# Performance work log

Measured on AMD Instinct MI355X. Metric: run time of the kernel, lower is better.

Reference implementation:

```python
import jax, jax.numpy as jnp
import numpy as np

N = 50000      # num_nodes
E = 300000     # edges per edge type
T = 3          # num_edge_type
C = 2          # num_channels
F_IN = 64      # feature_size
HID = 64       # hidden_size (w_out)
NL = 2         # num_layers (GT layers per FastGTN)
BETA = 0.5     # gtn_beta
TP = 0.8       # teleport_probability


def setup_inputs() -> dict:
    key = jax.random.key(0)
    ks = jax.random.split(key, 16)
    X = jax.random.normal(ks[0], (N, F_IN), dtype=jnp.float32)
    edge_index_0 = jax.random.randint(ks[1], (2, E), 0, N)
    edge_index_1 = jax.random.randint(ks[2], (2, E), 0, N)
    edge_index_2 = jax.random.randint(ks[3], (2, E), 0, N)
    edge_value_0 = jax.random.uniform(ks[4], (E,), dtype=jnp.float32)
    edge_value_1 = jax.random.uniform(ks[5], (E,), dtype=jnp.float32)
    edge_value_2 = jax.random.uniform(ks[6], (E,), dtype=jnp.float32)
    # glorot for Ws (per-channel projection), std=0.1 for GT layer mixing weights
    g0 = np.sqrt(6.0 / (F_IN + HID))
    g1 = np.sqrt(6.0 / (HID + HID))
    Ws0 = jax.random.uniform(ks[7], (C, F_IN, HID), minval=-g0, maxval=g0, dtype=jnp.float32)
    Ws1 = jax.random.uniform(ks[8], (C, HID, HID), minval=-g1, maxval=g1, dtype=jnp.float32)
    layerW0 = 0.1 * jax.random.normal(ks[9], (NL, C, T), dtype=jnp.float32)
    layerW1 = 0.1 * jax.random.normal(ks[10], (NL, C, T), dtype=jnp.float32)
    gl = np.sqrt(1.0 / (C * HID))
    lin_W0 = jax.random.uniform(ks[11], (C * HID, HID), minval=-gl, maxval=gl, dtype=jnp.float32)
    lin_b0 = jax.random.uniform(ks[12], (HID,), minval=-gl, maxval=gl, dtype=jnp.float32)
    lin_W1 = jax.random.uniform(ks[13], (C * HID, HID), minval=-gl, maxval=gl, dtype=jnp.float32)
    lin_b1 = jax.random.uniform(ks[14], (HID,), minval=-gl, maxval=gl, dtype=jnp.float32)
    return dict(X=X,
                edge_value_0=edge_value_0, edge_value_1=edge_value_1, edge_value_2=edge_value_2,
                Ws0=Ws0, Ws1=Ws1, layerW0=layerW0, layerW1=layerW1,
                lin_W0=lin_W0, lin_b0=lin_b0, lin_W1=lin_W1, lin_b1=lin_b1,
                edge_index_0=edge_index_0, edge_index_1=edge_index_1, edge_index_2=edge_index_2)


def _spmm_mix(H, filt, vals, etype, row, col):
    # H: [C, N, d]; filt: [C, T] softmaxed; vals: [Etot]; etype/row/col: [Etot]
    # == for each channel c: sum_j filt[c,j] * (A_j @ H[c])
    w = vals[None, :] * filt[:, etype]          # [C, Etot]
    msg = w[:, :, None] * H[:, col, :]          # [C, Etot, d]
    return jax.vmap(lambda m: jax.ops.segment_sum(m, row, num_segments=N))(msg)


def _fastgtn_block(Xin, Ws, layerW, linW, linb, row, col, vals, etype):
    H = jnp.einsum('nf,cfo->cno', Xin, Ws)      # [C, N, HID]
    X0 = jax.lax.stop_gradient(H)               # X_ = H.clone().detach()
    for l in range(NL):
        filt = jax.nn.softmax(layerW[l], axis=1)
        H = _spmm_mix(H, filt, vals, etype, row, col)
    Hm = TP * jax.nn.relu(BETA * X0 + (1.0 - BETA) * H) + (1.0 - TP) * X0
    Hm = jnp.transpose(Hm, (1, 0, 2)).reshape(N, C * Hm.shape[-1])  # [N, C*HID]
    return jax.nn.relu(Hm @ linW + linb)


def reference(X, edge_value_0, edge_value_1, edge_value_2,
              Ws0, Ws1, layerW0, layerW1,
              lin_W0, lin_b0, lin_W1, lin_b1,
              edge_index_0, edge_index_1, edge_index_2):
    row = jnp.concatenate([edge_index_0[0], edge_index_1[0], edge_index_2[0]])
    col = jnp.concatenate([edge_index_0[1], edge_index_1[1], edge_index_2[1]])
    vals = jnp.concatenate([edge_value_0, edge_value_1, edge_value_2])
    etype = jnp.repeat(jnp.arange(T), E)
    H = _fastgtn_block(X, Ws0, layerW0, lin_W0, lin_b0, row, col, vals, etype)
    H = _fastgtn_block(H, Ws1, layerW1, lin_W1, lin_b1, row, col, vals, etype)
    return H
```

## Files before the change

kernel.cpp:

```cpp
#include <hip/hip_runtime.h>
#include <hip/hip_fp16.h>

#define NN 50000
#define EE 300000
#define ETOT (3 * EE)
#define HD 64
#define RB 256
#define NB 196
#define BSTRIDE 6144


__global__ void filt_kernel(const float* __restrict__ lw0,
                            const float* __restrict__ lw1,
                            float* __restrict__ filt) {
    int i = threadIdx.x;
    if (i < 8) {
        int b = i >> 2, l = (i >> 1) & 1, c = i & 1;
        const float* lw = (b == 0 ? lw0 : lw1) + l * 6 + c * 3;
        float a0 = lw[0], a1 = lw[1], a2 = lw[2];
        float m  = fmaxf(a0, fmaxf(a1, a2));
        float e0 = expf(a0 - m), e1 = expf(a1 - m), e2 = expf(a2 - m);
        float s  = e0 + e1 + e2;
        float* o = filt + i * 3;
        o[0] = e0 / s; o[1] = e1 / s; o[2] = e2 / s;
    }
}

__global__ void __launch_bounds__(256)
bin_kernel(const int* __restrict__ ei0, const int* __restrict__ ei1,
           const int* __restrict__ ei2,
           const float* __restrict__ ev0, const float* __restrict__ ev1,
           const float* __restrict__ ev2,
           int* __restrict__ cursor, uint2* __restrict__ staged) {
    int t = blockIdx.y;
    const int*   ei = (t == 0) ? ei0 : (t == 1) ? ei1 : ei2;
    const float* ev = (t == 0) ? ev0 : (t == 1) ? ev1 : ev2;
    int e = blockIdx.x * 256 + threadIdx.x;
    if (e >= EE) return;
    int row = ei[e];
    int col = ei[EE + e];
    unsigned int q = (unsigned int)__float2int_rn(ev[e] * 16383.0f);
    unsigned int mw = (unsigned int)col | ((unsigned int)t << 16) | (q << 18);
    int b = row >> 8;
    int pos = atomicAdd(&cursor[b * 16], 1);
    staged[b * BSTRIDE + pos] = make_uint2(mw, (unsigned int)row);
}

__global__ void __launch_bounds__(256)
bscan_kernel(const int* __restrict__ cursor, int* __restrict__ bbase,
             int* __restrict__ rp) {
    __shared__ int wsum[4];
    int tid = threadIdx.x, lane = tid & 63, wv = tid >> 6;
    int v = (tid < NB) ? cursor[tid * 16] : 0;
    int x = v;
#pragma unroll
    for (int d = 1; d < 64; d <<= 1) {
        int y = __shfl_up(x, d);
        if (lane >= d) x += y;
    }
    if (lane == 63) wsum[wv] = x;
    __syncthreads();
    if (tid == 0) {
        int s = 0;
        for (int i = 0; i < 4; ++i) { int t = wsum[i]; wsum[i] = s; s += t; }
    }
    __syncthreads();
    x += wsum[wv];
    if (tid < NB) bbase[tid] = x - v;
    if (tid == 0) rp[NN] = ETOT;
}

__global__ void __launch_bounds__(256)
csr_kernel(const uint2* __restrict__ staged, const int* __restrict__ cursor,
           const int* __restrict__ bbase, int* __restrict__ rp,
           unsigned int* __restrict__ meta) {
    __shared__ int hist[RB];
    __shared__ int lcur[RB];
    __shared__ int wsum[4];
    __shared__ unsigned int metaL[BSTRIDE];
    int b   = blockIdx.x;
    int tid = threadIdx.x;
    int cnt  = cursor[b * 16];
    int base = bbase[b];
    int row0 = b * RB;

    hist[tid] = 0;
    __syncthreads();
    for (int i = tid; i < cnt; i += 256) {
        uint2 s = staged[b * BSTRIDE + i];
        atomicAdd(&hist[(int)s.y - row0], 1);
    }
    __syncthreads();
    int lane = tid & 63, wv = tid >> 6;
    int v = hist[tid];
    int x = v;
#pragma unroll
    for (int d = 1; d < 64; d <<= 1) {
        int y = __shfl_up(x, d);
        if (lane >= d) x += y;
    }
    if (lane == 63) wsum[wv] = x;
    __syncthreads();
    if (tid == 0) {
        int s = 0;
        for (int i = 0; i < 4; ++i) { int t = wsum[i]; wsum[i] = s; s += t; }
    }
    __syncthreads();
    int excl = x + wsum[wv] - v;
    lcur[tid] = excl;
    int row = row0 + tid;
    if (row < NN) rp[row] = base + excl;
    __syncthreads();
    for (int i = tid; i < cnt; i += 256) {
        uint2 s = staged[b * BSTRIDE + i];
        int p = atomicAdd(&lcur[(int)s.y - row0], 1);
        metaL[p] = s.x;
    }
    __syncthreads();
    for (int i = tid; i < cnt; i += 256)
        meta[base + i] = metaL[i];
}

#define PROJ_NTILE (NN / 16)
__global__ void __launch_bounds__(256)
proj_kernel(const float* __restrict__ Xin, const float* __restrict__ Ws,
            __half2* __restrict__ Hh) {
    __shared__ float Wl[2 * 64 * 64];
    __shared__ float Xs[16 * 65];
    int tid = threadIdx.x;
    for (int i = tid; i < 2 * 64 * 64; i += 256) Wl[i] = Ws[i];
    int oq = (tid & 15) * 4;
    int ln = tid >> 4;
    for (int tile = blockIdx.x; tile < PROJ_NTILE; tile += gridDim.x) {
        int n0 = tile * 16;
        __syncthreads();
        for (int i = tid; i < 16 * 64; i += 256)
            Xs[(i >> 6) * 65 + (i & 63)] = Xin[(n0 + (i >> 6)) * 64 + (i & 63)];
        __syncthreads();
        float a0[4] = {0.f, 0.f, 0.f, 0.f};
        float a1[4] = {0.f, 0.f, 0.f, 0.f};
        for (int f = 0; f < 64; ++f) {
            float  x  = Xs[ln * 65 + f];
            float4 w0 = *(const float4*)&Wl[f * 64 + oq];
            float4 w1 = *(const float4*)&Wl[4096 + f * 64 + oq];
            a0[0] += x * w0.x; a0[1] += x * w0.y;
            a0[2] += x * w0.z; a0[3] += x * w0.w;
            a1[0] += x * w1.x; a1[1] += x * w1.y;
            a1[2] += x * w1.z; a1[3] += x * w1.w;
        }
        float4 o4;
        ((__half2*)&o4)[0] = __floats2half2_rn(a0[0], a1[0]);
        ((__half2*)&o4)[1] = __floats2half2_rn(a0[1], a1[1]);
        ((__half2*)&o4)[2] = __floats2half2_rn(a0[2], a1[2]);
        ((__half2*)&o4)[3] = __floats2half2_rn(a0[3], a1[3]);
        *(float4*)&Hh[(n0 + ln) * HD + oq] = o4;
    }
}

__global__ void __launch_bounds__(256)
spmm_kernel(const float4* __restrict__ Hin4, float4* __restrict__ Hout4,
            const unsigned int* __restrict__ meta, const int* __restrict__ rp,
            const float* __restrict__ filt ) {
    const int wid  = threadIdx.x >> 6;
    const int lane = threadIdx.x & 63;
    const int g    = lane >> 4;
    const int fq   = lane & 15;
    const int row  = blockIdx.x * 4 + wid;

    const float s = 1.0f / 16383.0f;
    const float F00 = filt[0] * s, F01 = filt[1] * s, F02 = filt[2] * s;
    const float F10 = filt[3] * s, F11 = filt[4] * s, F12 = filt[5] * s;

    float accA[4] = {0.f, 0.f, 0.f, 0.f};
    float accB[4] = {0.f, 0.f, 0.f, 0.f};

    const int beg = rp[row], end = rp[row + 1];
    for (int j0 = beg; j0 < end; j0 += 64) {
        int cnt = min(end - j0, 64);
        unsigned int m = (lane < cnt) ? meta[j0 + lane] : 0u;
        for (int k = 0; k < cnt; k += 8) {
            unsigned int mmA = (unsigned int)__shfl((int)m, k + g);
            unsigned int mmB = (unsigned int)__shfl((int)m, k + 4 + g);
            float4 rA = Hin4[(mmA & 0xffffu) * 16 + fq];
            float4 rB = Hin4[(mmB & 0xffffu) * 16 + fq];
            int   etA = (mmA >> 16) & 3,  etB = (mmB >> 16) & 3;
            float qA  = (float)(mmA >> 18), qB = (float)(mmB >> 18);
            float w0A = qA * ((etA == 0) ? F00 : (etA == 1) ? F01 : F02);
            float w1A = qA * ((etA == 0) ? F10 : (etA == 1) ? F11 : F12);
            float w0B = qB * ((etB == 0) ? F00 : (etB == 1) ? F01 : F02);
            float w1B = qB * ((etB == 0) ? F10 : (etB == 1) ? F11 : F12);
#pragma unroll
            for (int i = 0; i < 4; ++i) {
                float2 xA = __half22float2(((const __half2*)&rA)[i]);
                float2 xB = __half22float2(((const __half2*)&rB)[i]);
                accA[i] += w0A * xA.x + w0B * xB.x;
                accB[i] += w1A * xA.y + w1B * xB.y;
            }
        }
    }
#pragma unroll
    for (int i = 0; i < 4; ++i) {
        accA[i] += __shfl_xor(accA[i], 16); accA[i] += __shfl_xor(accA[i], 32);
        accB[i] += __shfl_xor(accB[i], 16); accB[i] += __shfl_xor(accB[i], 32);
    }
    if (g == 0) {
        float4 o4;
        ((__half2*)&o4)[0] = __floats2half2_rn(accA[0], accB[0]);
        ((__half2*)&o4)[1] = __floats2half2_rn(accA[1], accB[1]);
        ((__half2*)&o4)[2] = __floats2half2_rn(accA[2], accB[2]);
        ((__half2*)&o4)[3] = __floats2half2_rn(accA[3], accB[3]);
        Hout4[row * 16 + fq] = o4;
    }
}

#define EPI_TILE 64
#define HS_STRIDE 132
__global__ void __launch_bounds__(256)
epilogue_kernel(const __half2* __restrict__ X0, const __half2* __restrict__ H,
                const float* __restrict__ linW, const float* __restrict__ linb,
                float* __restrict__ out) {
    __shared__ float Wl[128 * 64];
    __shared__ float Hs[EPI_TILE * HS_STRIDE];
    int tid = threadIdx.x;
    for (int i = tid; i < 128 * 64; i += 256) Wl[i] = linW[i];
    int oq = tid & 15, nq = tid >> 4;
    float bias[4];
#pragma unroll
    for (int i = 0; i < 4; ++i) bias[i] = linb[oq + 16 * i];
    const int ntiles = (NN + EPI_TILE - 1) / EPI_TILE;
    for (int tile = blockIdx.x; tile < ntiles; tile += gridDim.x) {
        int n0 = tile * EPI_TILE;
        __syncthreads();
        for (int i = tid; i < EPI_TILE * 64; i += 256) {
            int ln = i >> 6, d = i & 63;
            int n = n0 + ln;
            float2 x0 = make_float2(0.f, 0.f), h = make_float2(0.f, 0.f);
            if (n < NN) {
                x0 = __half22float2(X0[n * HD + d]);
                h  = __half22float2(H [n * HD + d]);
            }
            float z0 = fmaxf(0.5f * x0.x + 0.5f * h.x, 0.f);
            float z1 = fmaxf(0.5f * x0.y + 0.5f * h.y, 0.f);
            Hs[ln * HS_STRIDE + d]      = 0.8f * z0 + 0.2f * x0.x;
            Hs[ln * HS_STRIDE + 64 + d] = 0.8f * z1 + 0.2f * x0.y;
        }
        __syncthreads();
        float acc[4][4];
#pragma unroll
        for (int j = 0; j < 4; ++j)
#pragma unroll
            for (int i = 0; i < 4; ++i) acc[j][i] = bias[i];
        for (int k = 0; k < 128; k += 4) {
            float4 hq[4];
#pragma unroll
            for (int j = 0; j < 4; ++j)
                hq[j] = *(const float4*)&Hs[(nq + 16 * j) * HS_STRIDE + k];
#pragma unroll
            for (int kk = 0; kk < 4; ++kk) {
                float w[4];
#pragma unroll
                for (int i = 0; i < 4; ++i) w[i] = Wl[(k + kk) * 64 + oq + 16 * i];
#pragma unroll
                for (int j = 0; j < 4; ++j) {
                    float x = (kk == 0) ? hq[j].x : (kk == 1) ? hq[j].y
                             : (kk == 2) ? hq[j].z : hq[j].w;
#pragma unroll
                    for (int i = 0; i < 4; ++i) acc[j][i] += x * w[i];
                }
            }
        }
#pragma unroll
        for (int j = 0; j < 4; ++j) {
            int n = n0 + nq + 16 * j;
            if (n < NN) {
#pragma unroll
                for (int i = 0; i < 4; ++i)
                    out[n * HD + oq + 16 * i] = fmaxf(acc[j][i], 0.f);
            }
        }
    }
}

extern "C" void kernel_launch(void* const* d_in, const int* in_sizes, int n_in,
                              void* d_out, int out_size, void* d_ws, size_t ws_size,
                              hipStream_t stream) {
    const float* X     = (const float*)d_in[0];
    const float* ev0   = (const float*)d_in[1];
    const float* ev1   = (const float*)d_in[2];
    const float* ev2   = (const float*)d_in[3];
    const float* Ws0   = (const float*)d_in[4];
    const float* Ws1   = (const float*)d_in[5];
    const float* lw0   = (const float*)d_in[6];
    const float* lw1   = (const float*)d_in[7];
    const float* linW0 = (const float*)d_in[8];
    const float* linb0 = (const float*)d_in[9];
    const float* linW1 = (const float*)d_in[10];
    const float* linb1 = (const float*)d_in[11];
    const int*   ei0   = (const int*)d_in[12];
    const int*   ei1   = (const int*)d_in[13];
    const int*   ei2   = (const int*)d_in[14];
    float* out = (float*)d_out;

    float* ws = (float*)d_ws;
    __half2* X0h = (__half2*)(ws);
    __half2* Ha  = (__half2*)(ws + 1 * NN * HD);
    __half2* Hb  = (__half2*)(ws + 2 * NN * HD);
    float*   mid = ws + 3 * NN * HD;
    uint2*   staged = (uint2*)mid;
    float*   filt   = ws + 4 * NN * HD;
    int*     cursor = (int*)(filt + 32);
    int*     bbase  = cursor + NB * 16;
    int*     rp     = bbase + 256;
    unsigned int* meta = (unsigned int*)(rp + NN + 16);

    filt_kernel<<<1, 64, 0, stream>>>(lw0, lw1, filt);
    hipMemsetAsync(cursor, 0, NB * 16 * sizeof(int), stream);
    dim3 egrid((EE + 255) / 256, 3);
    bin_kernel<<<egrid, 256, 0, stream>>>(ei0, ei1, ei2, ev0, ev1, ev2,
                                          cursor, staged);
    bscan_kernel<<<1, 256, 0, stream>>>(cursor, bbase, rp);
    csr_kernel<<<NB, 256, 0, stream>>>(staged, cursor, bbase, rp, meta);

    proj_kernel<<<512, 256, 0, stream>>>(X, Ws0, X0h);
    spmm_kernel<<<NN / 4, 256, 0, stream>>>((const float4*)X0h, (float4*)Ha,
                                            meta, rp, filt + 0);
    spmm_kernel<<<NN / 4, 256, 0, stream>>>((const float4*)Ha, (float4*)Hb,
                                            meta, rp, filt + 6);
    epilogue_kernel<<<512, 256, 0, stream>>>(X0h, Hb, linW0, linb0, mid);

    proj_kernel<<<512, 256, 0, stream>>>(mid, Ws1, X0h);
    spmm_kernel<<<NN / 4, 256, 0, stream>>>((const float4*)X0h, (float4*)Ha,
                                            meta, rp, filt + 12);
    spmm_kernel<<<NN / 4, 256, 0, stream>>>((const float4*)Ha, (float4*)Hb,
                                            meta, rp, filt + 18);
    epilogue_kernel<<<512, 256, 0, stream>>>(X0h, Hb, linW1, linb1, out);
}
```

Baseline: 443.0 us.

## Replace global-atomic edge binning with two-pass per-chunk histogram and scan

```diff
diff --git a/kernel.cpp b/kernel.cpp
--- a/kernel.cpp
+++ b/kernel.cpp
@@ -7,7 +7,12 @@
 #define HD 64
 #define RB 256
 #define NB 196
-#define BSTRIDE 6144
+#define CHUNK 8192
+#define NBLKT ((EE + CHUNK - 1) / CHUNK)
+#define NBT (3 * NBLKT)
+#define NTOT (NB * NBT)
+#define GS_VPT ((NTOT + 1023) / 1024)
+#define MAXB 6144
 
 
 __global__ void filt_kernel(const float* __restrict__ lw0,
@@ -27,67 +32,109 @@
 }
 
 __global__ void __launch_bounds__(256)
-bin_kernel(const int* __restrict__ ei0, const int* __restrict__ ei1,
-           const int* __restrict__ ei2,
-           const float* __restrict__ ev0, const float* __restrict__ ev1,
-           const float* __restrict__ ev2,
-           int* __restrict__ cursor, uint2* __restrict__ staged) {
+hist1_kernel(const int* __restrict__ ei0, const int* __restrict__ ei1,
+             const int* __restrict__ ei2, int* __restrict__ hist) {
+    __shared__ int lh[NB];
+    int t = blockIdx.y;
+    const int* ei = (t == 0) ? ei0 : (t == 1) ? ei1 : ei2;
+    int tid = threadIdx.x;
+    for (int i = tid; i < NB; i += 256) lh[i] = 0;
+    __syncthreads();
+    int e0 = blockIdx.x * CHUNK;
+    for (int it = 0; it < CHUNK / 256; ++it) {
+        int e = e0 + it * 256 + tid;
+        if (e < EE) atomicAdd(&lh[ei[e] >> 8], 1);
+    }
+    __syncthreads();
+    int flat = t * NBLKT + blockIdx.x;
+    for (int i = tid; i < NB; i += 256) hist[flat * NB + i] = lh[i];
+}
+
+__global__ void __launch_bounds__(1024)
+gscan_kernel(const int* __restrict__ hist, int* __restrict__ gbase,
+             int* __restrict__ bbase, int* __restrict__ rp) {
+    __shared__ int wsum[16];
+    int tid = threadIdx.x, lane = tid & 63, wv = tid >> 6;
+    int s0 = tid * GS_VPT;
+    int local = 0;
+    for (int j = 0; j < GS_VPT; ++j) {
+        int s = s0 + j;
+        if (s < NTOT) {
+            int bucket = s / NBT, flat = s - bucket * NBT;
+            local += hist[flat * NB + bucket];
+        }
+    }
+    int x = local;
+#pragma unroll
+    for (int d = 1; d < 64; d <<= 1) {
+        int y = __shfl_up(x, d);
+        if (lane >= d) x += y;
+    }
+    if (lane == 63) wsum[wv] = x;
+    __syncthreads();
+    if (tid == 0) {
+        int s = 0;
+        for (int i = 0; i < 16; ++i) { int t = wsum[i]; wsum[i] = s; s += t; }
+    }
+    __syncthreads();
+    int run = x + wsum[wv] - local;
+    for (int j = 0; j < GS_VPT; ++j) {
+        int s = s0 + j;
+        if (s < NTOT) {
+            int bucket = s / NBT, flat = s - bucket * NBT;
+            gbase[flat * NB + bucket] = run;
+            if (flat == 0) bbase[bucket] = run;
+            run += hist[flat * NB + bucket];
+        }
+    }
+    if (tid == 0) { bbase[NB] = ETOT; rp[NN] = ETOT; }
+}
+
+__global__ void __launch_bounds__(256)
+place_kernel(const int* __restrict__ ei0, const int* __restrict__ ei1,
+             const int* __restrict__ ei2,
+             const float* __restrict__ ev0, const float* __restrict__ ev1,
+             const float* __restrict__ ev2,
+             const int* __restrict__ gbase, uint2* __restrict__ staged) {
+    __shared__ int lbase[NB];
     int t = blockIdx.y;
     const int*   ei = (t == 0) ? ei0 : (t == 1) ? ei1 : ei2;
     const float* ev = (t == 0) ? ev0 : (t == 1) ? ev1 : ev2;
-    int e = blockIdx.x * 256 + threadIdx.x;
-    if (e >= EE) return;
-    int row = ei[e];
-    int col = ei[EE + e];
-    unsigned int q = (unsigned int)__float2int_rn(ev[e] * 16383.0f);
-    unsigned int mw = (unsigned int)col | ((unsigned int)t << 16) | (q << 18);
-    int b = row >> 8;
-    int pos = atomicAdd(&cursor[b * 16], 1);
-    staged[b * BSTRIDE + pos] = make_uint2(mw, (unsigned int)row);
-}
-
-__global__ void __launch_bounds__(256)
-bscan_kernel(const int* __restrict__ cursor, int* __restrict__ bbase,
-             int* __restrict__ rp) {
-    __shared__ int wsum[4];
-    int tid = threadIdx.x, lane = tid & 63, wv = tid >> 6;
-    int v = (tid < NB) ? cursor[tid * 16] : 0;
-    int x = v;
-#pragma unroll
-    for (int d = 1; d < 64; d <<= 1) {
-        int y = __shfl_up(x, d);
-        if (lane >= d) x += y;
-    }
-    if (lane == 63) wsum[wv] = x;
-    __syncthreads();
-    if (tid == 0) {
-        int s = 0;
-        for (int i = 0; i < 4; ++i) { int t = wsum[i]; wsum[i] = s; s += t; }
-    }
-    __syncthreads();
-    x += wsum[wv];
-    if (tid < NB) bbase[tid] = x - v;
-    if (tid == 0) rp[NN] = ETOT;
-}
-
-__global__ void __launch_bounds__(256)
-csr_kernel(const uint2* __restrict__ staged, const int* __restrict__ cursor,
-           const int* __restrict__ bbase, int* __restrict__ rp,
-           unsigned int* __restrict__ meta) {
+    int tid = threadIdx.x;
+    int flat = t * NBLKT + blockIdx.x;
+    for (int i = tid; i < NB; i += 256) lbase[i] = gbase[flat * NB + i];
+    __syncthreads();
+    int e0 = blockIdx.x * CHUNK;
+    for (int it = 0; it < CHUNK / 256; ++it) {
+        int e = e0 + it * 256 + tid;
+        if (e < EE) {
+            int row = ei[e];
+            int col = ei[EE + e];
+            unsigned int q = (unsigned int)__float2int_rn(ev[e] * 16383.0f);
+            unsigned int mw = (unsigned int)col | ((unsigned int)t << 16) | (q << 18);
+            int pos = atomicAdd(&lbase[row >> 8], 1);
+            staged[pos] = make_uint2(mw, (unsigned int)row);
+        }
+    }
+}
+
+__global__ void __launch_bounds__(256)
+csr_kernel(const uint2* __restrict__ staged, const int* __restrict__ bbase,
+           int* __restrict__ rp, unsigned int* __restrict__ meta) {
     __shared__ int hist[RB];
     __shared__ int lcur[RB];
     __shared__ int wsum[4];
-    __shared__ unsigned int metaL[BSTRIDE];
+    __shared__ unsigned int metaL[MAXB];
     int b   = blockIdx.x;
     int tid = threadIdx.x;
-    int cnt  = cursor[b * 16];
     int base = bbase[b];
+    int cnt  = bbase[b + 1] - base;
     int row0 = b * RB;
 
     hist[tid] = 0;
     __syncthreads();
     for (int i = tid; i < cnt; i += 256) {
-        uint2 s = staged[b * BSTRIDE + i];
+        uint2 s = staged[base + i];
         atomicAdd(&hist[(int)s.y - row0], 1);
     }
     __syncthreads();
@@ -112,7 +159,7 @@
     if (row < NN) rp[row] = base + excl;
     __syncthreads();
     for (int i = tid; i < cnt; i += 256) {
-        uint2 s = staged[b * BSTRIDE + i];
+        uint2 s = staged[base + i];
         int p = atomicAdd(&lcur[(int)s.y - row0], 1);
         metaL[p] = s.x;
     }
@@ -308,18 +355,19 @@
     float*   mid = ws + 3 * NN * HD;
     uint2*   staged = (uint2*)mid;
     float*   filt   = ws + 4 * NN * HD;
-    int*     cursor = (int*)(filt + 32);
-    int*     bbase  = cursor + NB * 16;
-    int*     rp     = bbase + 256;
+    int*     hist   = (int*)(filt + 32);
+    int*     gbase  = hist + NTOT;
+    int*     bbase  = gbase + NTOT;
+    int*     rp     = bbase + NB + 4;
     unsigned int* meta = (unsigned int*)(rp + NN + 16);
 
     filt_kernel<<<1, 64, 0, stream>>>(lw0, lw1, filt);
-    hipMemsetAsync(cursor, 0, NB * 16 * sizeof(int), stream);
-    dim3 egrid((EE + 255) / 256, 3);
-    bin_kernel<<<egrid, 256, 0, stream>>>(ei0, ei1, ei2, ev0, ev1, ev2,
-                                          cursor, staged);
-    bscan_kernel<<<1, 256, 0, stream>>>(cursor, bbase, rp);
-    csr_kernel<<<NB, 256, 0, stream>>>(staged, cursor, bbase, rp, meta);
+    dim3 egrid(NBLKT, 3);
+    hist1_kernel<<<egrid, 256, 0, stream>>>(ei0, ei1, ei2, hist);
+    gscan_kernel<<<1, 1024, 0, stream>>>(hist, gbase, bbase, rp);
+    place_kernel<<<egrid, 256, 0, stream>>>(ei0, ei1, ei2, ev0, ev1, ev2,
+                                            gbase, staged);
+    csr_kernel<<<NB, 256, 0, stream>>>(staged, bbase, rp, meta);
 
     proj_kernel<<<512, 256, 0, stream>>>(X, Ws0, X0h);
     spmm_kernel<<<NN / 4, 256, 0, stream>>>((const float4*)X0h, (float4*)Ha,
```

Measured after the change: 414.5 us. 1.07x faster.
